# Kernel tuning notes

Hardware: AMD Instinct MI355X
Metric: run time of the kernel (lower is better)

Reference implementation:

```python
import jax, jax.numpy as jnp
import numpy as np

B, S, H, D = 4, 4096, 8, 128
EPS = 1e-6


def layernorm(x, g, b, axes):
    m = jnp.mean(x, axis=axes, keepdims=True)
    v = jnp.mean(jnp.square(x - m), axis=axes, keepdims=True)
    return (x - m) / jnp.sqrt(v + EPS) * g + b


def setup_inputs() -> dict:
    key = jax.random.key(0)
    ks = jax.random.split(key, 6)
    scale = 0.05
    return {
        "heads_input": jax.random.normal(ks[0], (B, S, H, D), jnp.float32),
        # GroupLinear trans_hid: per-head (2D -> 3D)
        "W_hid": jax.random.normal(ks[1], (H, 2 * D, 3 * D), jnp.float32) * scale,
        "b_hid": jax.random.normal(ks[2], (H, 3 * D), jnp.float32) * scale,
        # GroupLinear trans_og: per-head (2D -> D)
        "W_og": jax.random.normal(ks[3], (H, 2 * D, D), jnp.float32) * scale,
        "b_og": jax.random.normal(ks[4], (H, D), jnp.float32) * scale,
        # LayerNorm affine params (elementwise_affine=True)
        "ln_csum_g": jnp.ones((H, D), jnp.float32),
        "ln_csum_b": jnp.zeros((H, D), jnp.float32),
        "ln_hid_g": jnp.ones((H, 3, D), jnp.float32),
        "ln_hid_b": jnp.zeros((H, 3, D), jnp.float32),
        "ln_og_g": jnp.ones((H, D), jnp.float32),
        "ln_og_b": jnp.zeros((H, D), jnp.float32),
        "init_cx": jnp.zeros((1, H, D), jnp.float32),
    }


def reference(heads_input, W_hid, b_hid, W_og, b_og, ln_csum_g, ln_csum_b,
              ln_hid_g, ln_hid_b, ln_og_g, ln_og_b, init_cx):
    b, s, h, d = heads_input.shape
    # shifted cumulative sum over time, then LayerNorm over (head, dim)
    shifted = jnp.concatenate(
        [jnp.zeros((b, 1, h, d), heads_input.dtype), heads_input[:, :-1]], axis=1)
    csum = layernorm(jnp.cumsum(shifted, axis=1), ln_csum_g, ln_csum_b, (-2, -1))
    cat = jnp.concatenate([heads_input, csum], axis=-1)        # [b,s,h,2d]
    hid = jnp.einsum('bshi,hio->bsho', cat, W_hid) + b_hid     # [b,s,h,3d]
    hid = layernorm(hid.reshape(b, s, h, 3, d), ln_hid_g, ln_hid_b, (-3, -2, -1))
    igate, fgate, hidden = hid[..., 0, :], hid[..., 1, :], hid[..., 2, :]
    fgate = jax.nn.sigmoid(fgate)
    igh = jax.nn.sigmoid(igate) * jax.nn.relu(hidden)
    # LGateFunc: cell_t = fgate_t * cell_{t-1} + igh_t, cell_0 = init_cx
    c0 = jnp.broadcast_to(init_cx, (b, h, d)).astype(heads_input.dtype)
    def step(c, fi):
        f, i = fi
        c = f * c + i
        return c, c
    _, cells = jax.lax.scan(step, c0,
                            (fgate.transpose(1, 0, 2, 3), igh.transpose(1, 0, 2, 3)))
    cell = cells.transpose(1, 0, 2, 3)                          # [b,s,h,d]
    og_in = jnp.concatenate([heads_input, cell], axis=-1)       # [b,s,h,2d]
    og = layernorm(jnp.einsum('bshi,hio->bsho', og_in, W_og) + b_og,
                   ln_og_g, ln_og_b, (-2, -1))
    return jax.nn.sigmoid(og) * cell
```

## Files before the change

kernel.cpp:

```cpp
#include <hip/hip_runtime.h>

#define EPSF 1e-6f


typedef __attribute__((ext_vector_type(8))) short short8v;
typedef __attribute__((ext_vector_type(4))) float float4v;

__device__ __forceinline__ float sigm(float x) { return 1.0f / (1.0f + __expf(-x)); }

__device__ __forceinline__ unsigned short f2bf(float f) {
    unsigned int u = __float_as_uint(f);
    u = (u + 0x7fffu + ((u >> 16) & 1u)) >> 16;
    return (unsigned short)u;
}
__device__ __forceinline__ float bf2f(unsigned short s) { return __uint_as_float(((unsigned int)s) << 16); }
__device__ __forceinline__ float bf2f_lo(unsigned int p) { return __uint_as_float(p << 16); }
__device__ __forceinline__ float bf2f_hi(unsigned int p) { return __uint_as_float(p & 0xffff0000u); }
__device__ __forceinline__ unsigned int pack2bf(float a, float b) {
    return (unsigned int)f2bf(a) | ((unsigned int)f2bf(b) << 16);
}

__device__ __forceinline__ void block_reduce2(float& a, float& b) {
#pragma unroll
    for (int off = 32; off > 0; off >>= 1) {
        a += __shfl_down(a, off);
        b += __shfl_down(b, off);
    }
    __shared__ float sa[8], sb[8];
    int wid = threadIdx.x >> 6;
    int lane = threadIdx.x & 63;
    if (lane == 0) { sa[wid] = a; sb[wid] = b; }
    __syncthreads();
    a = sa[0] + sa[1] + sa[2] + sa[3];
    b = sb[0] + sb[1] + sb[2] + sb[3];
}

__global__ __launch_bounds__(256) void k_prep_w(const float* __restrict__ W, unsigned short* __restrict__ Wt,
                                                int Nw) {
    int idx = blockIdx.x * 256 + threadIdx.x;
    int k = idx & 255;
    int rest = idx >> 8;
    int o = rest % Nw;
    int h = rest / Nw;
    Wt[idx] = f2bf(W[((size_t)h * 256 + k) * Nw + o]);
}

__global__ __launch_bounds__(256) void k_cumsum_a(const float* __restrict__ X, float* __restrict__ cS,
                                                  unsigned short* __restrict__ XB) {
    int t = blockIdx.x * 256 + threadIdx.x;
    int d = t & 127, h = (t >> 7) & 7, k = (t >> 10) & 63, b = t >> 16;
    size_t base = (((size_t)(b * 4096 + k * 64)) * 8 + h) * 128 + d;
    float s = 0.f;
    for (int j = 0; j < 64; ++j) {
        unsigned short xb = f2bf(X[base + (size_t)j * 1024]);
        XB[base + (size_t)j * 1024] = xb;
        s += bf2f(xb);
    }
    cS[(size_t)((b * 8 + h) * 128 + d) * 64 + k] = s;
}

__global__ __launch_bounds__(256) void k_cumsum_b(const float* __restrict__ cS, float* __restrict__ cO) {
    int ch = blockIdx.x * 256 + threadIdx.x;
    size_t base = (size_t)ch * 64;
    float off = 0.f;
    for (int k = 0; k < 64; ++k) { float v = cS[base + k]; cO[base + k] = off; off += v; }
}

__global__ __launch_bounds__(256) void k_cumsum_c(const unsigned short* __restrict__ XB,
                                                  const float* __restrict__ cO,
                                                  unsigned short* __restrict__ CSUMB) {
    int t = blockIdx.x * 256 + threadIdx.x;
    int d = t & 127, h = (t >> 7) & 7, k = (t >> 10) & 63, b = t >> 16;
    int ch = (b * 8 + h) * 128 + d;
    float run = cO[(size_t)ch * 64 + k];
    size_t base = (((size_t)(b * 4096 + k * 64)) * 8 + h) * 128 + d;
    for (int j = 0; j < 64; ++j) {
        float x = bf2f(XB[base + (size_t)j * 1024]);
        CSUMB[base + (size_t)j * 1024] = f2bf(run);
        run += x;
    }
}

__global__ __launch_bounds__(256) void k_ln_csum(const unsigned short* __restrict__ CSUMB,
                                                 unsigned short* __restrict__ CSB,
                                                 const float* __restrict__ g, const float* __restrict__ bb) {
    int bs = blockIdx.x, t = threadIdx.x;
    uint2 u = ((const uint2*)(CSUMB + (size_t)bs * 1024))[t];
    float4 v;
    v.x = bf2f_lo(u.x); v.y = bf2f_hi(u.x);
    v.z = bf2f_lo(u.y); v.w = bf2f_hi(u.y);
    float s = v.x + v.y + v.z + v.w;
    float ss = v.x * v.x + v.y * v.y + v.z * v.z + v.w * v.w;
    block_reduce2(s, ss);
    float m = s * (1.f / 1024.f);
    float var = ss * (1.f / 1024.f) - m * m;
    float r = rsqrtf(fmaxf(var, 0.f) + EPSF);
    float4 gv = ((const float4*)g)[t];
    float4 bv = ((const float4*)bb)[t];
    uint2 o;
    o.x = pack2bf((v.x - m) * r * gv.x + bv.x, (v.y - m) * r * gv.y + bv.y);
    o.y = pack2bf((v.z - m) * r * gv.z + bv.z, (v.w - m) * r * gv.w + bv.w);
    ((uint2*)(CSB + (size_t)bs * 1024))[t] = o;
}

__global__ __launch_bounds__(256) void k_gemm_bf16(const unsigned short* __restrict__ A1,
                                                   const unsigned short* __restrict__ A2,
                                                   const unsigned short* __restrict__ Wt,
                                                   const float* __restrict__ bias,
                                                   unsigned short* __restrict__ OUT, int Nw, int m0,
                                                   int nbx) {
    __shared__ short As[2][8192];
    __shared__ short Bs[2][8192];
    int bid = blockIdx.x;
    int h = bid & 7;
    int rest = bid >> 3;
    int bx = rest % nbx;
    int by = rest / nbx;
    int t0 = threadIdx.x;
    int lane = t0 & 63, wid = t0 >> 6;
    int wr = wid >> 1, wc = wid & 1;
    int l15 = lane & 15, l4 = lane >> 4;
    int lr = lane >> 3, lc = lane & 7;
    const int bxc = bx * 128;
    const size_t mbase = (size_t)(m0 + by * 128);

    float4v acc[4][4];
#pragma unroll
    for (int i = 0; i < 4; ++i)
#pragma unroll
        for (int j = 0; j < 4; ++j) acc[i][j] = (float4v)(0.f);

    auto STAGE = [&](int t, int buf) {
        const unsigned short* src = (t < 2) ? A1 : A2;
        int kofs = (t & 1) * 64;
#pragma unroll
        for (int it = 0; it < 4; ++it) {
            int r0 = wid * 32 + it * 8;
            int r = r0 + lr;
            int c = lc ^ (r & 7);
            size_t g = ((mbase + r) * 8 + h) * 128 + kofs + c * 8;
            __builtin_amdgcn_global_load_lds((const __attribute__((address_space(1))) void*)(src + g),
                                             (__attribute__((address_space(3))) void*)(&As[buf][r0 * 64]),
                                             16, 0, 0);
        }
#pragma unroll
        for (int it = 0; it < 4; ++it) {
            int n0 = wid * 32 + it * 8;
            int cl = n0 + lr;
            int c = lc ^ (cl & 7);
            size_t g = ((size_t)(h * Nw + bxc + cl)) * 256 + t * 64 + c * 8;
            __builtin_amdgcn_global_load_lds((const __attribute__((address_space(1))) void*)(Wt + g),
                                             (__attribute__((address_space(3))) void*)(&Bs[buf][n0 * 64]),
                                             16, 0, 0);
        }
    };

    STAGE(0, 0);
#pragma unroll
    for (int t = 0; t < 4; ++t) {
        int cur = t & 1;
        if (t < 3) STAGE(t + 1, cur ^ 1);
        if (t < 3) asm volatile("s_waitcnt vmcnt(8)" ::: "memory");
        else       asm volatile("s_waitcnt vmcnt(0)" ::: "memory");
        __builtin_amdgcn_s_barrier();
        __builtin_amdgcn_sched_barrier(0);
#pragma unroll
        for (int kk = 0; kk < 2; ++kk) {
            short8v a[4], b[4];
#pragma unroll
            for (int i = 0; i < 4; ++i) {
                int r = wr * 64 + i * 16 + l15;
                int slot = (kk * 4 + l4) ^ (r & 7);
                a[i] = *(const short8v*)(&As[cur][r * 64 + slot * 8]);
            }
#pragma unroll
            for (int j = 0; j < 4; ++j) {
                int c = wc * 64 + j * 16 + l15;
                int slot = (kk * 4 + l4) ^ (c & 7);
                b[j] = *(const short8v*)(&Bs[cur][c * 64 + slot * 8]);
            }
#pragma unroll
            for (int i = 0; i < 4; ++i)
#pragma unroll
                for (int j = 0; j < 4; ++j)
                    acc[i][j] = __builtin_amdgcn_mfma_f32_16x16x32_bf16(a[i], b[j], acc[i][j], 0, 0, 0);
        }
        __builtin_amdgcn_sched_barrier(0);
        __builtin_amdgcn_s_barrier();
    }
#pragma unroll
    for (int j = 0; j < 4; ++j) {
        int o = bxc + wc * 64 + j * 16 + l15;
        float bv = bias[h * Nw + o];
#pragma unroll
        for (int i = 0; i < 4; ++i) {
            int mlb = by * 128 + wr * 64 + i * 16 + l4 * 4;
#pragma unroll
            for (int q = 0; q < 4; ++q) {
                OUT[((size_t)(mlb + q) * 8 + h) * Nw + o] = f2bf(acc[i][j][q] + bv);
            }
        }
    }
}

__global__ __launch_bounds__(256) void k_ln_gates(const unsigned short* __restrict__ HID,
                                                  unsigned short* __restrict__ FG,
                                                  unsigned short* __restrict__ IG,
                                                  const float* __restrict__ g, const float* __restrict__ bb,
                                                  int m0) {
    __shared__ float sm[3072];
    int bsl = blockIdx.x, t = threadIdx.x;
    int bs = m0 + bsl;
    const uint4* row = (const uint4*)(HID + (size_t)bsl * 3072);
    float s = 0.f, ss = 0.f;
    for (int idx = t; idx < 384; idx += 256) {
        uint4 u = row[idx];
        float f0 = bf2f_lo(u.x), f1 = bf2f_hi(u.x);
        float f2 = bf2f_lo(u.y), f3 = bf2f_hi(u.y);
        float f4 = bf2f_lo(u.z), f5 = bf2f_hi(u.z);
        float f6 = bf2f_lo(u.w), f7 = bf2f_hi(u.w);
        float* p = sm + idx * 8;
        p[0] = f0; p[1] = f1; p[2] = f2; p[3] = f3; p[4] = f4; p[5] = f5; p[6] = f6; p[7] = f7;
        s += f0 + f1 + f2 + f3 + f4 + f5 + f6 + f7;
        ss += f0 * f0 + f1 * f1 + f2 * f2 + f3 * f3 + f4 * f4 + f5 * f5 + f6 * f6 + f7 * f7;
    }
    block_reduce2(s, ss);
    float m = s * (1.f / 3072.f);
    float var = ss * (1.f / 3072.f) - m * m;
    float r = rsqrtf(fmaxf(var, 0.f) + EPSF);
    int u0 = t * 4;
    int h = u0 >> 7;
    int d0 = u0 & 127;
    float fr[4], ir[4];
#pragma unroll
    for (int q = 0; q < 4; ++q) {
        int d = d0 + q;
        float yi = sm[h * 384 + d];
        float yf = sm[h * 384 + 128 + d];
        float yh = sm[h * 384 + 256 + d];
        float ni = (yi - m) * r * g[(h * 3 + 0) * 128 + d] + bb[(h * 3 + 0) * 128 + d];
        float nf = (yf - m) * r * g[(h * 3 + 1) * 128 + d] + bb[(h * 3 + 1) * 128 + d];
        float nh = (yh - m) * r * g[(h * 3 + 2) * 128 + d] + bb[(h * 3 + 2) * 128 + d];
        fr[q] = sigm(nf);
        ir[q] = sigm(ni) * fmaxf(nh, 0.f);
    }
    uint2 fo, io;
    fo.x = pack2bf(fr[0], fr[1]); fo.y = pack2bf(fr[2], fr[3]);
    io.x = pack2bf(ir[0], ir[1]); io.y = pack2bf(ir[2], ir[3]);
    ((uint2*)(FG + (size_t)bs * 1024))[t] = fo;
    ((uint2*)(IG + (size_t)bs * 1024))[t] = io;
}

__global__ __launch_bounds__(256) void k_scan_a(const unsigned short* __restrict__ FG,
                                                const unsigned short* __restrict__ IG,
                                                float* __restrict__ cF, float* __restrict__ cC) {
    int t = blockIdx.x * 256 + threadIdx.x;
    int d2 = t & 63, h = (t >> 6) & 7, k = (t >> 9) & 63, b = t >> 15;
    size_t base = (((size_t)(b * 4096 + k * 64)) * 8 + h) * 64 + d2;
    const unsigned int* FGu = (const unsigned int*)FG;
    const unsigned int* IGu = (const unsigned int*)IG;
    float F0 = 1.f, C0 = 0.f, F1 = 1.f, C1 = 0.f;
    for (int j = 0; j < 64; ++j) {
        unsigned int fg = FGu[base + (size_t)j * 512];
        unsigned int ig = IGu[base + (size_t)j * 512];
        float f0 = bf2f_lo(fg), f1 = bf2f_hi(fg);
        C0 = fmaf(f0, C0, bf2f_lo(ig)); F0 *= f0;
        C1 = fmaf(f1, C1, bf2f_hi(ig)); F1 *= f1;
    }
    size_t ci0 = ((size_t)((b * 8 + h) * 128 + d2 * 2)) * 64 + k;
    cF[ci0] = F0; cC[ci0] = C0;
    cF[ci0 + 64] = F1; cC[ci0 + 64] = C1;
}

__global__ __launch_bounds__(256) void k_scan_b(const float* __restrict__ cF, const float* __restrict__ cC,
                                                const float* __restrict__ initcx, float* __restrict__ cI) {
    int ch = blockIdx.x * 256 + threadIdx.x;
    float c = initcx[ch & 1023];
    size_t base = (size_t)ch * 64;
    for (int k = 0; k < 64; ++k) {
        cI[base + k] = c;
        c = fmaf(cF[base + k], c, cC[base + k]);
    }
}

__global__ __launch_bounds__(256) void k_scan_c(const unsigned short* __restrict__ FG,
                                                unsigned short* __restrict__ IGCLB,
                                                const float* __restrict__ cI) {
    int t = blockIdx.x * 256 + threadIdx.x;
    int d2 = t & 63, h = (t >> 6) & 7, k = (t >> 9) & 63, b = t >> 15;
    size_t base = (((size_t)(b * 4096 + k * 64)) * 8 + h) * 64 + d2;
    const unsigned int* FGu = (const unsigned int*)FG;
    unsigned int* IGu = (unsigned int*)IGCLB;
    size_t ci0 = ((size_t)((b * 8 + h) * 128 + d2 * 2)) * 64 + k;
    float c0 = cI[ci0], c1 = cI[ci0 + 64];
    for (int j = 0; j < 64; ++j) {
        unsigned int fg = FGu[base + (size_t)j * 512];
        unsigned int ig = IGu[base + (size_t)j * 512];
        c0 = fmaf(bf2f_lo(fg), c0, bf2f_lo(ig));
        c1 = fmaf(bf2f_hi(fg), c1, bf2f_hi(ig));
        IGu[base + (size_t)j * 512] = pack2bf(c0, c1);
    }
}

__global__ __launch_bounds__(256) void k_ln_out(const unsigned short* __restrict__ OG,
                                                const unsigned short* __restrict__ CLB,
                                                const float* __restrict__ g, const float* __restrict__ bb,
                                                float* __restrict__ OUT, int m0) {
    int bsl = blockIdx.x, t = threadIdx.x;
    int bs = m0 + bsl;
    uint2 u = ((const uint2*)(OG + (size_t)bsl * 1024))[t];
    float4 v;
    v.x = bf2f_lo(u.x); v.y = bf2f_hi(u.x);
    v.z = bf2f_lo(u.y); v.w = bf2f_hi(u.y);
    float s = v.x + v.y + v.z + v.w;
    float ss = v.x * v.x + v.y * v.y + v.z * v.z + v.w * v.w;
    block_reduce2(s, ss);
    float m = s * (1.f / 1024.f);
    float var = ss * (1.f / 1024.f) - m * m;
    float r = rsqrtf(fmaxf(var, 0.f) + EPSF);
    float4 gv = ((const float4*)g)[t];
    float4 bv = ((const float4*)bb)[t];
    uint2 cu = ((const uint2*)(CLB + (size_t)bs * 1024))[t];
    float4 cv;
    cv.x = bf2f_lo(cu.x); cv.y = bf2f_hi(cu.x);
    cv.z = bf2f_lo(cu.y); cv.w = bf2f_hi(cu.y);
    float4 o;
    o.x = sigm((v.x - m) * r * gv.x + bv.x) * cv.x;
    o.y = sigm((v.y - m) * r * gv.y + bv.y) * cv.y;
    o.z = sigm((v.z - m) * r * gv.z + bv.z) * cv.z;
    o.w = sigm((v.w - m) * r * gv.w + bv.w) * cv.w;
    ((float4*)(OUT + (size_t)bs * 1024))[t] = o;
}

extern "C" void kernel_launch(void* const* d_in, const int* in_sizes, int n_in,
                              void* d_out, int out_size, void* d_ws, size_t ws_size,
                              hipStream_t stream) {
    const float* X      = (const float*)d_in[0];
    const float* W_hid  = (const float*)d_in[1];
    const float* b_hid  = (const float*)d_in[2];
    const float* W_og   = (const float*)d_in[3];
    const float* b_og   = (const float*)d_in[4];
    const float* g_cs   = (const float*)d_in[5];
    const float* b_cs   = (const float*)d_in[6];
    const float* g_hid  = (const float*)d_in[7];
    const float* b_hidl = (const float*)d_in[8];
    const float* g_og   = (const float*)d_in[9];
    const float* b_ogl  = (const float*)d_in[10];
    const float* initcx = (const float*)d_in[11];

    float* ws = (float*)d_ws;
    const size_t O_SC    = 0ull;
    const size_t O_XB    = 1310720ull;
    const size_t O_CSUMB = 9699328ull;
    const size_t O_CSB   = 18087936ull;
    const size_t O_IGB   = 26476544ull;
    const size_t O_WTH   = 34865152ull;
    const size_t O_WTO   = 35258368ull;
    const size_t O_HID   = 35389440ull;

    float* cS = ws + O_SC;
    float* cO = cS + 262144;
    float* cF = cO + 262144;
    float* cC = cF + 262144;
    float* cI = cC + 262144;
    unsigned short* XB    = (unsigned short*)(ws + O_XB);
    unsigned short* CSUMB = (unsigned short*)(ws + O_CSUMB);
    unsigned short* FGB   = CSUMB;
    unsigned short* CSB   = (unsigned short*)(ws + O_CSB);
    unsigned short* IGB   = (unsigned short*)(ws + O_IGB);
    unsigned short* CLB   = IGB;
    unsigned short* WTH   = (unsigned short*)(ws + O_WTH);
    unsigned short* WTO   = (unsigned short*)(ws + O_WTO);
    unsigned short* HIDC  = (unsigned short*)(ws + O_HID);

    size_t avail = (ws_size / 4 > O_HID) ? ws_size / 4 - O_HID : 0;
    int CH = 1024;
    for (int c = 16384; c >= 1024; c >>= 1) {
        if ((size_t)c * 1536ull <= avail) { CH = c; break; }
    }
    const int NC = 16384 / CH;

    dim3 blk(256);
    k_prep_w<<<3072, blk, 0, stream>>>(W_hid, WTH, 384);
    k_prep_w<<<1024, blk, 0, stream>>>(W_og, WTO, 128);
    k_cumsum_a<<<1024, blk, 0, stream>>>(X, cS, XB);
    k_cumsum_b<<<16, blk, 0, stream>>>(cS, cO);
    k_cumsum_c<<<1024, blk, 0, stream>>>(XB, cO, CSUMB);
    k_ln_csum<<<16384, blk, 0, stream>>>(CSUMB, CSB, g_cs, b_cs);
    for (int c = 0; c < NC; ++c) {
        int m0 = c * CH;
        k_gemm_bf16<<<8 * 3 * (CH / 128), blk, 0, stream>>>(XB, CSB, WTH, b_hid, HIDC, 384, m0, 3);
        k_ln_gates<<<CH, blk, 0, stream>>>(HIDC, FGB, IGB, g_hid, b_hidl, m0);
    }
    k_scan_a<<<512, blk, 0, stream>>>(FGB, IGB, cF, cC);
    k_scan_b<<<16, blk, 0, stream>>>(cF, cC, initcx, cI);
    k_scan_c<<<512, blk, 0, stream>>>(FGB, IGB, cI);
    for (int c = 0; c < NC; ++c) {
        int m0 = c * CH;
        k_gemm_bf16<<<8 * 1 * (CH / 128), blk, 0, stream>>>(XB, CLB, WTO, b_og, HIDC, 128, m0, 1);
        k_ln_out<<<CH, blk, 0, stream>>>(HIDC, CLB, g_og, b_ogl, (float*)d_out, m0);
    }
}
```

Baseline: 242.0 us.

## Parallelize chunk-carry scans with wave shuffles and widen GEMM to 512 threads

The serial per-channel carry scans (cumsum offsets and gate-scan initial states) are replaced with wave-level Hillis-Steele shuffle scans, and their launches grow from 16 to 1024 blocks. This removes a 64-step serial dependency that ran on very few threads. The GEMM now uses 512 threads with 8 waves that each compute 32x64, and it preloads all four K stages into 64KB of LDS up front, dropping the double-buffer trailing barrier. This costs more LDS per block and may lower occupancy. The shuffle scans reorder floating-point operations, so the carry values may differ slightly from the serial version.

```diff
diff --git a/kernel.cpp b/kernel.cpp
--- a/kernel.cpp
+++ b/kernel.cpp
@@ -60,10 +60,17 @@
 }
 
 __global__ __launch_bounds__(256) void k_cumsum_b(const float* __restrict__ cS, float* __restrict__ cO) {
-    int ch = blockIdx.x * 256 + threadIdx.x;
-    size_t base = (size_t)ch * 64;
-    float off = 0.f;
-    for (int k = 0; k < 64; ++k) { float v = cS[base + k]; cO[base + k] = off; off += v; }
+    int wave = (blockIdx.x * 256 + threadIdx.x) >> 6;
+    int lane = threadIdx.x & 63;
+    size_t idx = (size_t)wave * 64 + lane;
+    float v = cS[idx];
+    float incl = v;
+#pragma unroll
+    for (int d = 1; d < 64; d <<= 1) {
+        float t = __shfl_up(incl, d);
+        if (lane >= d) incl += t;
+    }
+    cO[idx] = incl - v;
 }
 
 __global__ __launch_bounds__(256) void k_cumsum_c(const unsigned short* __restrict__ XB,
@@ -103,14 +110,14 @@
     ((uint2*)(CSB + (size_t)bs * 1024))[t] = o;
 }
 
-__global__ __launch_bounds__(256) void k_gemm_bf16(const unsigned short* __restrict__ A1,
+__global__ __launch_bounds__(512) void k_gemm_bf16(const unsigned short* __restrict__ A1,
                                                    const unsigned short* __restrict__ A2,
                                                    const unsigned short* __restrict__ Wt,
                                                    const float* __restrict__ bias,
                                                    unsigned short* __restrict__ OUT, int Nw, int m0,
                                                    int nbx) {
-    __shared__ short As[2][8192];
-    __shared__ short Bs[2][8192];
+    __shared__ short As[4][8192];
+    __shared__ short Bs[4][8192];
     int bid = blockIdx.x;
     int h = bid & 7;
     int rest = bid >> 3;
@@ -124,77 +131,76 @@
     const int bxc = bx * 128;
     const size_t mbase = (size_t)(m0 + by * 128);
 
-    float4v acc[4][4];
-#pragma unroll
-    for (int i = 0; i < 4; ++i)
+    float4v acc[2][4];
+#pragma unroll
+    for (int i = 0; i < 2; ++i)
 #pragma unroll
         for (int j = 0; j < 4; ++j) acc[i][j] = (float4v)(0.f);
 
-    auto STAGE = [&](int t, int buf) {
+    auto STAGE = [&](int t) {
         const unsigned short* src = (t < 2) ? A1 : A2;
         int kofs = (t & 1) * 64;
 #pragma unroll
-        for (int it = 0; it < 4; ++it) {
-            int r0 = wid * 32 + it * 8;
+        for (int it = 0; it < 2; ++it) {
+            int r0 = wid * 16 + it * 8;
             int r = r0 + lr;
             int c = lc ^ (r & 7);
             size_t g = ((mbase + r) * 8 + h) * 128 + kofs + c * 8;
             __builtin_amdgcn_global_load_lds((const __attribute__((address_space(1))) void*)(src + g),
-                                             (__attribute__((address_space(3))) void*)(&As[buf][r0 * 64]),
+                                             (__attribute__((address_space(3))) void*)(&As[t][r0 * 64]),
                                              16, 0, 0);
         }
 #pragma unroll
-        for (int it = 0; it < 4; ++it) {
-            int n0 = wid * 32 + it * 8;
+        for (int it = 0; it < 2; ++it) {
+            int n0 = wid * 16 + it * 8;
             int cl = n0 + lr;
             int c = lc ^ (cl & 7);
             size_t g = ((size_t)(h * Nw + bxc + cl)) * 256 + t * 64 + c * 8;
             __builtin_amdgcn_global_load_lds((const __attribute__((address_space(1))) void*)(Wt + g),
-                                             (__attribute__((address_space(3))) void*)(&Bs[buf][n0 * 64]),
+                                             (__attribute__((address_space(3))) void*)(&Bs[t][n0 * 64]),
                                              16, 0, 0);
         }
     };
 
-    STAGE(0, 0);
+    STAGE(0); STAGE(1); STAGE(2); STAGE(3);
+
 #pragma unroll
     for (int t = 0; t < 4; ++t) {
-        int cur = t & 1;
-        if (t < 3) STAGE(t + 1, cur ^ 1);
-        if (t < 3) asm volatile("s_waitcnt vmcnt(8)" ::: "memory");
-        else       asm volatile("s_waitcnt vmcnt(0)" ::: "memory");
+        if (t == 0)      asm volatile("s_waitcnt vmcnt(12)" ::: "memory");
+        else if (t == 1) asm volatile("s_waitcnt vmcnt(8)" ::: "memory");
+        else if (t == 2) asm volatile("s_waitcnt vmcnt(4)" ::: "memory");
+        else             asm volatile("s_waitcnt vmcnt(0)" ::: "memory");
         __builtin_amdgcn_s_barrier();
         __builtin_amdgcn_sched_barrier(0);
 #pragma unroll
         for (int kk = 0; kk < 2; ++kk) {
-            short8v a[4], b[4];
-#pragma unroll
-            for (int i = 0; i < 4; ++i) {
-                int r = wr * 64 + i * 16 + l15;
+            short8v a[2], b[4];
+#pragma unroll
+            for (int i = 0; i < 2; ++i) {
+                int r = wr * 32 + i * 16 + l15;
                 int slot = (kk * 4 + l4) ^ (r & 7);
-                a[i] = *(const short8v*)(&As[cur][r * 64 + slot * 8]);
+                a[i] = *(const short8v*)(&As[t][r * 64 + slot * 8]);
             }
 #pragma unroll
             for (int j = 0; j < 4; ++j) {
                 int c = wc * 64 + j * 16 + l15;
                 int slot = (kk * 4 + l4) ^ (c & 7);
-                b[j] = *(const short8v*)(&Bs[cur][c * 64 + slot * 8]);
+                b[j] = *(const short8v*)(&Bs[t][c * 64 + slot * 8]);
             }
 #pragma unroll
-            for (int i = 0; i < 4; ++i)
+            for (int i = 0; i < 2; ++i)
 #pragma unroll
                 for (int j = 0; j < 4; ++j)
                     acc[i][j] = __builtin_amdgcn_mfma_f32_16x16x32_bf16(a[i], b[j], acc[i][j], 0, 0, 0);
         }
-        __builtin_amdgcn_sched_barrier(0);
-        __builtin_amdgcn_s_barrier();
     }
 #pragma unroll
     for (int j = 0; j < 4; ++j) {
         int o = bxc + wc * 64 + j * 16 + l15;
         float bv = bias[h * Nw + o];
 #pragma unroll
-        for (int i = 0; i < 4; ++i) {
-            int mlb = by * 128 + wr * 64 + i * 16 + l4 * 4;
+        for (int i = 0; i < 2; ++i) {
+            int mlb = by * 128 + wr * 32 + i * 16 + l4 * 4;
 #pragma unroll
             for (int q = 0; q < 4; ++q) {
                 OUT[((size_t)(mlb + q) * 8 + h) * Nw + o] = f2bf(acc[i][j][q] + bv);
@@ -274,13 +280,21 @@
 
 __global__ __launch_bounds__(256) void k_scan_b(const float* __restrict__ cF, const float* __restrict__ cC,
                                                 const float* __restrict__ initcx, float* __restrict__ cI) {
-    int ch = blockIdx.x * 256 + threadIdx.x;
-    float c = initcx[ch & 1023];
-    size_t base = (size_t)ch * 64;
-    for (int k = 0; k < 64; ++k) {
-        cI[base + k] = c;
-        c = fmaf(cF[base + k], c, cC[base + k]);
-    }
+    int wave = (blockIdx.x * 256 + threadIdx.x) >> 6;
+    int lane = threadIdx.x & 63;
+    size_t idx = (size_t)wave * 64 + lane;
+    float F = cF[idx], C = cC[idx];
+#pragma unroll
+    for (int d = 1; d < 64; d <<= 1) {
+        float Fp = __shfl_up(F, d);
+        float Cp = __shfl_up(C, d);
+        if (lane >= d) { C = fmaf(Cp, F, C); F *= Fp; }
+    }
+    float Fe = __shfl_up(F, 1);
+    float Ce = __shfl_up(C, 1);
+    if (lane == 0) { Fe = 1.f; Ce = 0.f; }
+    float c0 = initcx[wave & 1023];
+    cI[idx] = fmaf(Fe, c0, Ce);
 }
 
 __global__ __launch_bounds__(256) void k_scan_c(const unsigned short* __restrict__ FG,
@@ -381,23 +395,24 @@
     const int NC = 16384 / CH;
 
     dim3 blk(256);
+    dim3 blkg(512);
     k_prep_w<<<3072, blk, 0, stream>>>(W_hid, WTH, 384);
     k_prep_w<<<1024, blk, 0, stream>>>(W_og, WTO, 128);
     k_cumsum_a<<<1024, blk, 0, stream>>>(X, cS, XB);
-    k_cumsum_b<<<16, blk, 0, stream>>>(cS, cO);
+    k_cumsum_b<<<1024, blk, 0, stream>>>(cS, cO);
     k_cumsum_c<<<1024, blk, 0, stream>>>(XB, cO, CSUMB);
     k_ln_csum<<<16384, blk, 0, stream>>>(CSUMB, CSB, g_cs, b_cs);
     for (int c = 0; c < NC; ++c) {
         int m0 = c * CH;
-        k_gemm_bf16<<<8 * 3 * (CH / 128), blk, 0, stream>>>(XB, CSB, WTH, b_hid, HIDC, 384, m0, 3);
+        k_gemm_bf16<<<8 * 3 * (CH / 128), blkg, 0, stream>>>(XB, CSB, WTH, b_hid, HIDC, 384, m0, 3);
         k_ln_gates<<<CH, blk, 0, stream>>>(HIDC, FGB, IGB, g_hid, b_hidl, m0);
     }
     k_scan_a<<<512, blk, 0, stream>>>(FGB, IGB, cF, cC);
-    k_scan_b<<<16, blk, 0, stream>>>(cF, cC, initcx, cI);
+    k_scan_b<<<1024, blk, 0, stream>>>(cF, cC, initcx, cI);
     k_scan_c<<<512, blk, 0, stream>>>(FGB, IGB, cI);
     for (int c = 0; c < NC; ++c) {
         int m0 = c * CH;
-        k_gemm_bf16<<<8 * 1 * (CH / 128), blk, 0, stream>>>(XB, CLB, WTO, b_og, HIDC, 128, m0, 1);
+        k_gemm_bf16<<<8 * 1 * (CH / 128), blkg, 0, stream>>>(XB, CLB, WTO, b_og, HIDC, 128, m0, 1);
         k_ln_out<<<CH, blk, 0, stream>>>(HIDC, CLB, g_og, b_ogl, (float*)d_out, m0);
     }
 }
```

Measured after the change: 242.5 us. About the same (+0.2%).
